# Kernel tuning notes

Measured on AMD Instinct MI355X. Metric: run time of the kernel, lower is better.

The kernel has to match this reference:

```python
import jax, jax.numpy as jnp
import numpy as np

B, L, D = 16384, 50, 64      # nodes, history length, embed_dim
NU, NI, NR = 100000, 100000, 5


def setup_inputs() -> dict:
    key = jax.random.key(0)
    ks = jax.random.split(key, 16)
    s = 0.05
    return {
        "nodes": jax.random.randint(ks[0], (B,), 0, NU),
        "history_uv": jax.random.randint(ks[1], (B, L), 0, NI),
        "history_r": jax.random.randint(ks[2], (B, L), 0, NR),
        "v2e_w": jax.random.normal(ks[3], (NI, D), jnp.float32) * s,
        "u2e_w": jax.random.normal(ks[4], (NU, D), jnp.float32) * s,
        "r2e_w": jax.random.normal(ks[5], (NR, D), jnp.float32) * s,
        "w_r1_w": jax.random.normal(ks[6], (2 * D, D), jnp.float32) * s,
        "w_r1_b": jnp.zeros((D,), jnp.float32),
        "w_r2_w": jax.random.normal(ks[7], (D, D), jnp.float32) * s,
        "w_r2_b": jnp.zeros((D,), jnp.float32),
        "att1_w": jax.random.normal(ks[8], (2 * D, D), jnp.float32) * s,
        "att1_b": jnp.zeros((D,), jnp.float32),
        "att2_w": jax.random.normal(ks[9], (D, D), jnp.float32) * s,
        "att2_b": jnp.zeros((D,), jnp.float32),
        "att3_w": jax.random.normal(ks[10], (D, 1), jnp.float32) * s,
        "att3_b": jnp.zeros((1,), jnp.float32),
    }


def reference(nodes, history_uv, history_r, v2e_w, u2e_w, r2e_w,
              w_r1_w, w_r1_b, w_r2_w, w_r2_b,
              att1_w, att1_b, att2_w, att2_b, att3_w, att3_b):
    # Gather neighbor (item) and rating embeddings: [B, L, D]
    e_uv = v2e_w[history_uv]
    e_r = r2e_w[history_r]
    uv_rep = u2e_w[nodes]                      # [B, D] self (user) embedding
    # 2-layer MLP on concatenated (item, rating) embeddings
    x = jnp.concatenate([e_uv, e_r], axis=-1)  # [B, L, 2D]
    h = jax.nn.relu(x @ w_r1_w + w_r1_b)
    o_history = jax.nn.relu(h @ w_r2_w + w_r2_b)  # [B, L, D]
    # Attention over neighbors (GraphRec Attention, dropout off in eval)
    a = jnp.concatenate(
        [o_history, jnp.broadcast_to(uv_rep[:, None, :], o_history.shape)], axis=-1)
    a = jax.nn.relu(a @ att1_w + att1_b)
    a = jax.nn.relu(a @ att2_w + att2_b)
    logits = (a @ att3_w + att3_b)[..., 0]     # [B, L]
    att = jax.nn.softmax(logits, axis=-1)      # softmax over history dim
    # Attention-weighted sum of neighbor representations
    return jnp.einsum('bl,bld->bd', att, o_history)  # [B, D]
```

## Files before the change

kernel.cpp:

```cpp
#include <hip/hip_runtime.h>
#include <math.h>

#define NB 16384
#define LH 50
#define D  64

#define TBF_OFF 49152
#define UB_OFF  65536
#define P1_OFF  4259840

typedef _Float16 half2v __attribute__((ext_vector_type(2)));
typedef _Float16 half8  __attribute__((ext_vector_type(8)));
typedef float    f32x16 __attribute__((ext_vector_type(16)));
typedef unsigned int u32;

#define MFMA(a, b, c) __builtin_amdgcn_mfma_f32_32x32x16_f16((a), (b), (c), 0, 0, 0)


__device__ __forceinline__ u32 pack2(float a, float b) {
    half2v h; h[0] = (_Float16)a; h[1] = (_Float16)b;
    return __builtin_bit_cast(u32, h);
}
__device__ __forceinline__ half8 mk8(u32 a, u32 b, u32 c, u32 d) {
    uint4 t = make_uint4(a, b, c, d);
    return __builtin_bit_cast(half8, t);
}
__device__ __forceinline__ half8 cvt8(const float* __restrict__ p) {
    float4 u = *(const float4*)p;
    float4 v = *(const float4*)(p + 4);
    return mk8(pack2(u.x, u.y), pack2(u.z, u.w), pack2(v.x, v.y), pack2(v.z, v.w));
}
__device__ __forceinline__ half8 addrelu8(half8 a, half8 r) {
    half8 s = a + r;
    #pragma unroll
    for (int j = 0; j < 8; ++j) s[j] = s[j] > (_Float16)0 ? s[j] : (_Float16)0;
    return s;
}

__device__ __forceinline__ void xform_tile(const f32x16& t, int hv, half8& f0, half8& f1) {
    u32 p[8], rp[8];
    #pragma unroll
    for (int q = 0; q < 8; ++q) p[q] = pack2(fmaxf(t[2*q], 0.f), fmaxf(t[2*q+1], 0.f));
    #pragma unroll
    for (int q = 0; q < 8; ++q) rp[q] = (u32)__shfl_xor((int)p[q], 32, 64);
    f0 = hv ? mk8(rp[2], rp[3], p[2], p[3]) : mk8(p[0], p[1], rp[0], rp[1]);
    f1 = hv ? mk8(rp[6], rp[7], p[6], p[7]) : mk8(p[4], p[5], rp[4], rp[5]);
}

__device__ __forceinline__ f32x16 ldbias(const float* __restrict__ tb, int hv, int mt) {
    const float4* p = (const float4*)tb + hv*8 + mt*4;
    f32x16 r;
    #pragma unroll
    for (int q = 0; q < 4; ++q) {
        float4 v = p[q];
        r[4*q] = v.x; r[4*q+1] = v.y; r[4*q+2] = v.z; r[4*q+3] = v.w;
    }
    return r;
}

__device__ __forceinline__ half8 mkw(const float* __restrict__ W, int ks, int mt,
                                     int hv, int m) {
    half8 r;
    #pragma unroll
    for (int j = 0; j < 8; ++j)
        r[j] = (_Float16)W[(ks*16 + hv*8 + j)*64 + mt*32 + m];
    return r;
}

__global__ __launch_bounds__(256) void prep_all(
    const int*   __restrict__ nodes,
    const float* __restrict__ v2e, const float* __restrict__ u2e,
    const float* __restrict__ r2e,
    const float* __restrict__ w1,  const float* __restrict__ b1,
    const float* __restrict__ w2,  const float* __restrict__ b2,
    const float* __restrict__ wa1, const float* __restrict__ ba1,
    const float* __restrict__ wa2, const float* __restrict__ ba2,
    const float* __restrict__ wa3,
    _Float16* __restrict__ wsh, float* __restrict__ tbf,
    float* __restrict__ UB, _Float16* __restrict__ P1h) {
    const int blk = blockIdx.x;
    const int lane = threadIdx.x & 63;
    const int n = lane & 31, hv = lane >> 5;

    if (blk < 782) {
        const int tile = blk*4 + (threadIdx.x >> 6);
        if (tile >= 3125) return;
        const int item = tile*32 + n;
        half8 bf[4];
        #pragma unroll
        for (int ks = 0; ks < 4; ++ks)
            bf[ks] = cvt8(v2e + (size_t)item*64 + ks*16 + hv*8);
        f32x16 a0, a1;
        #pragma unroll
        for (int q = 0; q < 16; ++q) { a0[q] = 0.f; a1[q] = 0.f; }
        #pragma unroll
        for (int ks = 0; ks < 4; ++ks) {
            a0 = MFMA(mkw(w1, ks, 0, hv, n), bf[ks], a0);
            a1 = MFMA(mkw(w1, ks, 1, hv, n), bf[ks], a1);
        }
        u32 dw[16];
        #pragma unroll
        for (int q = 0; q < 8; ++q) dw[q]     = pack2(a0[2*q], a0[2*q+1]);
        #pragma unroll
        for (int q = 0; q < 8; ++q) dw[8 + q] = pack2(a1[2*q], a1[2*q+1]);
        uint4* dst = (uint4*)(P1h + (size_t)item*64 + hv*32);
        dst[0] = make_uint4(dw[0],  dw[1],  dw[2],  dw[3]);
        dst[1] = make_uint4(dw[4],  dw[5],  dw[6],  dw[7]);
        dst[2] = make_uint4(dw[8],  dw[9],  dw[10], dw[11]);
        dst[3] = make_uint4(dw[12], dw[13], dw[14], dw[15]);
        return;
    }
    if (blk < 910) {
        const int tile = (blk - 782)*4 + (threadIdx.x >> 6);
        const int s = tile*32 + n;
        const int nid = nodes[s];
        half8 bf[4];
        #pragma unroll
        for (int ks = 0; ks < 4; ++ks)
            bf[ks] = cvt8(u2e + (size_t)nid*64 + ks*16 + hv*8);
        f32x16 a0, a1;
        #pragma unroll
        for (int q = 0; q < 16; ++q) {
            a0[q] = ba1[(q & 3) + 8*(q >> 2) + 4*hv];
            a1[q] = ba1[32 + (q & 3) + 8*(q >> 2) + 4*hv];
        }
        const float* wup = wa1 + 64*64;
        #pragma unroll
        for (int ks = 0; ks < 4; ++ks) {
            a0 = MFMA(mkw(wup, ks, 0, hv, n), bf[ks], a0);
            a1 = MFMA(mkw(wup, ks, 1, hv, n), bf[ks], a1);
        }
        float4* dst = (float4*)(UB + (size_t)s*64 + hv*32);
        #pragma unroll
        for (int q = 0; q < 4; ++q) {
            dst[q]     = make_float4(a0[4*q], a0[4*q+1], a0[4*q+2], a0[4*q+3]);
            dst[4 + q] = make_float4(a1[4*q], a1[4*q+1], a1[4*q+2], a1[4*q+3]);
        }
        return;
    }
    if (blk < 958) {
        const int idx = (blk - 910)*256 + threadIdx.x;
        const int j = idx & 7, l2 = (idx >> 3) & 63;
        const int hv2 = l2 >> 5, m31 = l2 & 31;
        const int f = (idx >> 9) & 7, ks = f & 3, mt = f >> 2;
        const int sec = idx >> 12;
        const int tau = ks*16 + hv2*8 + j;
        float v;
        if (sec == 0) {
            const int thv = (tau >> 5) & 1, tmt = (tau >> 4) & 1, i = tau & 15;
            const int feat = tmt*32 + (i & 3) + 8*(i >> 2) + 4*thv;
            v = w2[feat*64 + mt*32 + m31];
        }
        else if (sec == 1) v = wa1[tau*64 + mt*32 + m31];
        else               v = wa2[tau*64 + mt*32 + m31];
        wsh[idx] = (_Float16)v;
        return;
    }
    if (blk == 958) {
        if (threadIdx.x < 64) {
            const int t = threadIdx.x;
            const int thv = t >> 5, r = t & 31, mtt = r >> 4, i = r & 15;
            const int feat = mtt*32 + (i & 3) + 8*(i >> 2) + 4*thv;
            tbf[t]       = b2[feat];
            tbf[64 + t]  = ba2[feat];
            tbf[128 + t] = wa3[feat];
        }
        return;
    }
    {
        _Float16* R1h = (_Float16*)(tbf + 192);
        #pragma unroll 1
        for (int base = 0; base < 320; base += 256) {
            const int o = base + (int)threadIdx.x;
            if (o < 320) {
                const int rr = o >> 6, tt = o & 63;
                const int thv = tt >> 5, r5 = tt & 31, mtt = r5 >> 4, i = r5 & 15;
                const int feat = mtt*32 + (i & 3) + 8*(i >> 2) + 4*thv;
                float acc = b1[feat];
                for (int k = 0; k < 64; ++k)
                    acc += r2e[rr*64 + k] * w1[(64 + k)*64 + feat];
                R1h[rr*64 + tt] = (_Float16)acc;
            }
        }
    }
}

__global__ __launch_bounds__(256, 4) void uv_main(
    const int*   __restrict__ huv,
    const int*   __restrict__ hr,
    const _Float16* __restrict__ P1h,
    const float* __restrict__ UB,
    const _Float16* __restrict__ wsh,
    const float* __restrict__ tbf,
    float*       __restrict__ out) {
    __shared__ float4 stage[4][520];
    const int lane = threadIdx.x & 63;
    const int w = threadIdx.x >> 6;
    const int b = blockIdx.x * 4 + w;
    const int n = lane & 31, hv = lane >> 5;
    float4* const stg = stage[w];

    #define G8(base, f) (*(const half8*)(wsh + (base) + (size_t)((f)*64 + lane)*8))

    const int tg = lane >> 3;
    const int qq = lane & 7;
    int rowid[8];
    #pragma unroll
    for (int j = 0; j < 8; ++j) {
        int t = j*8 + tg; if (t > LH-1) t = LH-1;
        rowid[j] = huv[b*LH + t];
    }
    float4 c[8];
    #pragma unroll
    for (int j = 0; j < 8; ++j)
        c[j] = *(const float4*)(P1h + (size_t)rowid[j]*64 + qq*8);

    const _Float16* R1h = (const _Float16*)(tbf + 192);
    const int t1  = (32 + n < LH) ? 32 + n : LH - 1;
    const int ir0 = __builtin_nontemporal_load(hr + b*LH + n);
    const int ir1 = __builtin_nontemporal_load(hr + b*LH + t1);

    #pragma unroll
    for (int j = 0; j < 8; ++j) stg[qq*65 + j*8 + tg] = c[j];

    half8 bf[2][4];
    #pragma unroll
    for (int ks = 0; ks < 4; ++ks) {
        half8 r0 = *(const half8*)(R1h + ir0*64 + ks*16 + hv*8);
        half8 r1 = *(const half8*)(R1h + ir1*64 + ks*16 + hv*8);
        bf[0][ks] = addrelu8(*(const half8*)&stg[(2*ks + hv)*65 + n],      r0);
        bf[1][ks] = addrelu8(*(const half8*)&stg[(2*ks + hv)*65 + 32 + n], r1);
    }

    half8 of[2][4];
    #pragma unroll
    for (int mt = 0; mt < 2; ++mt) {
        f32x16 a0 = ldbias(tbf, hv, mt);
        f32x16 a1 = ldbias(tbf, hv, mt);
        #pragma unroll
        for (int ks = 0; ks < 4; ++ks) {
            half8 wv = G8(0, mt*4 + ks);
            a0 = MFMA(wv, bf[0][ks], a0);
            a1 = MFMA(wv, bf[1][ks], a1);
        }
        xform_tile(a0, hv, of[0][mt*2], of[0][mt*2 + 1]);
        xform_tile(a1, hv, of[1][mt*2], of[1][mt*2 + 1]);
    }

    const float* ubrow = UB + (size_t)b * 64;
    half8 af[2][4];
    #pragma unroll
    for (int mt = 0; mt < 2; ++mt) {
        f32x16 a0 = ldbias(ubrow, hv, mt);
        f32x16 a1 = ldbias(ubrow, hv, mt);
        #pragma unroll
        for (int ks = 0; ks < 4; ++ks) {
            half8 wv = G8(4096, mt*4 + ks);
            a0 = MFMA(wv, of[0][ks], a0);
            a1 = MFMA(wv, of[1][ks], a1);
        }
        xform_tile(a0, hv, af[0][mt*2], af[0][mt*2 + 1]);
        xform_tile(a1, hv, af[1][mt*2], af[1][mt*2 + 1]);
    }

    float lg0 = 0.f, lg1 = 0.f;
    #pragma unroll
    for (int mt = 0; mt < 2; ++mt) {
        f32x16 c0, c1v;
        {
            const f32x16 bc = ldbias(tbf + 64, hv, mt);
            half8 wv = G8(8192, mt*4 + 0);
            c0  = MFMA(wv, af[0][0], bc);
            c1v = MFMA(wv, af[1][0], bc);
        }
        #pragma unroll
        for (int ks = 1; ks < 4; ++ks) {
            half8 wv = G8(8192, mt*4 + ks);
            c0  = MFMA(wv, af[0][ks], c0);
            c1v = MFMA(wv, af[1][ks], c1v);
        }
        #pragma unroll
        for (int q = 0; q < 4; ++q) {
            float4 w3 = ((const float4*)(tbf + 128))[hv*8 + mt*4 + q];
            lg0 += fmaxf(c0[4*q], 0.f)*w3.x + fmaxf(c0[4*q+1], 0.f)*w3.y
                 + fmaxf(c0[4*q+2], 0.f)*w3.z + fmaxf(c0[4*q+3], 0.f)*w3.w;
            lg1 += fmaxf(c1v[4*q], 0.f)*w3.x + fmaxf(c1v[4*q+1], 0.f)*w3.y
                 + fmaxf(c1v[4*q+2], 0.f)*w3.z + fmaxf(c1v[4*q+3], 0.f)*w3.w;
        }
    }
    lg0 += __shfl_xor(lg0, 32, 64);
    lg1 += __shfl_xor(lg1, 32, 64);
    if (32 + n >= LH) lg1 = -1e30f;

    float mx = fmaxf(lg0, lg1);
    #pragma unroll
    for (int off = 16; off >= 1; off >>= 1) mx = fmaxf(mx, __shfl_xor(mx, off, 64));
    const float e0 = __expf(lg0 - mx);
    const float e1 = __expf(lg1 - mx);
    float s = e0 + e1;
    #pragma unroll
    for (int off = 16; off >= 1; off >>= 1) s += __shfl_xor(s, off, 64);
    const float at0 = e0 / s, at1 = e1 / s;

    float cur[32];
    #pragma unroll
    for (int ks = 0; ks < 4; ++ks)
        #pragma unroll
        for (int j = 0; j < 8; ++j)
            cur[ks*8 + j] = at0 * (float)of[0][ks][j] + at1 * (float)of[1][ks][j];
    #pragma unroll
    for (int k = 0; k < 5; ++k) {
        const int d = 1 << k, mybit = (lane >> k) & 1, half = 16 >> k;
        #pragma unroll
        for (int j2 = 0; j2 < 16; ++j2) {
            if (j2 < half) {
                float sel  = mybit ? cur[2*j2]     : cur[2*j2 + 1];
                float got  = __shfl_xor(sel, d, 64);
                float keep = mybit ? cur[2*j2 + 1] : cur[2*j2];
                cur[j2] = keep + got;
            }
        }
    }
    const int feat = ((lane >> 3) & 3)*16 + hv*8 + (lane & 7);
    __builtin_nontemporal_store(cur[0], out + (size_t)b * D + feat);
    #undef G8
}

extern "C" void kernel_launch(void* const* d_in, const int* in_sizes, int n_in,
                              void* d_out, int out_size, void* d_ws, size_t ws_size,
                              hipStream_t stream) {
    const int*   nodes      = (const int*)  d_in[0];
    const int*   history_uv = (const int*)  d_in[1];
    const int*   history_r  = (const int*)  d_in[2];
    const float* v2e        = (const float*)d_in[3];
    const float* u2e        = (const float*)d_in[4];
    const float* r2e        = (const float*)d_in[5];
    const float* w1         = (const float*)d_in[6];
    const float* b1         = (const float*)d_in[7];
    const float* w2         = (const float*)d_in[8];
    const float* b2         = (const float*)d_in[9];
    const float* wa1        = (const float*)d_in[10];
    const float* ba1        = (const float*)d_in[11];
    const float* wa2        = (const float*)d_in[12];
    const float* ba2        = (const float*)d_in[13];
    const float* wa3        = (const float*)d_in[14];
    float* out = (float*)d_out;

    _Float16* wsh = (_Float16*)d_ws;
    float*    tbf = (float*)((char*)d_ws + TBF_OFF);
    float*    UB  = (float*)((char*)d_ws + UB_OFF);
    _Float16* P1h = (_Float16*)((char*)d_ws + P1_OFF);

    prep_all<<<960, 256, 0, stream>>>(nodes, v2e, u2e, r2e, w1, b1, w2, b2,
                                      wa1, ba1, wa2, ba2, wa3, wsh, tbf, UB, P1h);
    uv_main<<<NB/4, 256, 0, stream>>>(history_uv, history_r,
                                      P1h, UB, wsh, tbf, out);
}
```

Measured before the change: 197.4 us.

## Stage weights and bias tables in LDS and gather item rows directly

Each block now copies the fp16 MLP/attention weights, bias/att3 vectors and the rating-embedding table into shared memory once, then reads them from LDS instead of global memory. The cooperative row gather through a padded LDS staging buffer is replaced by per-lane direct half8 loads of the P1 rows in MFMA fragment layout. Launch bounds are raised to 6 blocks per SM to allow more occupancy. The trade-off is a per-block prologue copy and a __syncthreads, plus less coalesced gather loads (16-byte per-lane reads scattered across rows) and tighter register limits.

```diff
diff --git a/kernel.cpp b/kernel.cpp
--- a/kernel.cpp
+++ b/kernel.cpp
@@ -47,7 +47,7 @@
     f1 = hv ? mk8(rp[6], rp[7], p[6], p[7]) : mk8(p[4], p[5], rp[4], rp[5]);
 }
 
-__device__ __forceinline__ f32x16 ldbias(const float* __restrict__ tb, int hv, int mt) {
+__device__ __forceinline__ f32x16 ldbias(const float* tb, int hv, int mt) {
     const float4* p = (const float4*)tb + hv*8 + mt*4;
     f32x16 r;
     #pragma unroll
@@ -185,7 +185,7 @@
     }
 }
 
-__global__ __launch_bounds__(256, 4) void uv_main(
+__global__ __launch_bounds__(256, 6) void uv_main(
     const int*   __restrict__ huv,
     const int*   __restrict__ hr,
     const _Float16* __restrict__ P1h,
@@ -193,50 +193,50 @@
     const _Float16* __restrict__ wsh,
     const float* __restrict__ tbf,
     float*       __restrict__ out) {
-    __shared__ float4 stage[4][520];
-    const int lane = threadIdx.x & 63;
-    const int w = threadIdx.x >> 6;
+    __shared__ _Float16 lw[12288];
+    __shared__ float    ltb[192];
+    __shared__ _Float16 lr1[320];
+    const int tid = threadIdx.x;
+
+    {
+        const uint4* src = (const uint4*)wsh;
+        uint4* dst = (uint4*)lw;
+        #pragma unroll
+        for (int i = 0; i < 6; ++i) dst[tid + 256*i] = src[tid + 256*i];
+        if (tid < 48) ((uint4*)ltb)[tid] = ((const uint4*)tbf)[tid];
+        if (tid < 40) ((uint4*)lr1)[tid] = ((const uint4*)(tbf + 192))[tid];
+    }
+    __syncthreads();
+
+    const int lane = tid & 63;
+    const int w = tid >> 6;
     const int b = blockIdx.x * 4 + w;
     const int n = lane & 31, hv = lane >> 5;
-    float4* const stg = stage[w];
-
-    #define G8(base, f) (*(const half8*)(wsh + (base) + (size_t)((f)*64 + lane)*8))
-
-    const int tg = lane >> 3;
-    const int qq = lane & 7;
-    int rowid[8];
-    #pragma unroll
-    for (int j = 0; j < 8; ++j) {
-        int t = j*8 + tg; if (t > LH-1) t = LH-1;
-        rowid[j] = huv[b*LH + t];
-    }
-    float4 c[8];
-    #pragma unroll
-    for (int j = 0; j < 8; ++j)
-        c[j] = *(const float4*)(P1h + (size_t)rowid[j]*64 + qq*8);
-
-    const _Float16* R1h = (const _Float16*)(tbf + 192);
-    const int t1  = (32 + n < LH) ? 32 + n : LH - 1;
-    const int ir0 = __builtin_nontemporal_load(hr + b*LH + n);
-    const int ir1 = __builtin_nontemporal_load(hr + b*LH + t1);
-
-    #pragma unroll
-    for (int j = 0; j < 8; ++j) stg[qq*65 + j*8 + tg] = c[j];
+
+    #define G8(base, f) (*(const half8*)(lw + (base) + ((f)*64 + lane)*8))
+
+    const int t1   = (32 + n < LH) ? 32 + n : LH - 1;
+    const int row0 = huv[b*LH + n];
+    const int row1 = huv[b*LH + t1];
+    const int ir0  = hr[b*LH + n];
+    const int ir1  = hr[b*LH + t1];
 
     half8 bf[2][4];
     #pragma unroll
     for (int ks = 0; ks < 4; ++ks) {
-        half8 r0 = *(const half8*)(R1h + ir0*64 + ks*16 + hv*8);
-        half8 r1 = *(const half8*)(R1h + ir1*64 + ks*16 + hv*8);
-        bf[0][ks] = addrelu8(*(const half8*)&stg[(2*ks + hv)*65 + n],      r0);
-        bf[1][ks] = addrelu8(*(const half8*)&stg[(2*ks + hv)*65 + 32 + n], r1);
+        half8 p0 = *(const half8*)(P1h + (size_t)row0*64 + ks*16 + hv*8);
+        half8 p1 = *(const half8*)(P1h + (size_t)row1*64 + ks*16 + hv*8);
+        half8 r0 = *(const half8*)(lr1 + ir0*64 + ks*16 + hv*8);
+        half8 r1 = *(const half8*)(lr1 + ir1*64 + ks*16 + hv*8);
+        bf[0][ks] = addrelu8(p0, r0);
+        bf[1][ks] = addrelu8(p1, r1);
     }
 
     half8 of[2][4];
     #pragma unroll
     for (int mt = 0; mt < 2; ++mt) {
-        f32x16 a0 = ldbias(tbf, hv, mt);
-        f32x16 a1 = ldbias(tbf, hv, mt);
+        f32x16 a0 = ldbias(ltb, hv, mt);
+        f32x16 a1 = ldbias(ltb, hv, mt);
         #pragma unroll
         for (int ks = 0; ks < 4; ++ks) {
             half8 wv = G8(0, mt*4 + ks);
@@ -268,7 +268,7 @@
     for (int mt = 0; mt < 2; ++mt) {
         f32x16 c0, c1v;
         {
-            const f32x16 bc = ldbias(tbf + 64, hv, mt);
+            const f32x16 bc = ldbias(ltb + 64, hv, mt);
             half8 wv = G8(8192, mt*4 + 0);
             c0  = MFMA(wv, af[0][0], bc);
             c1v = MFMA(wv, af[1][0], bc);
@@ -281,7 +281,7 @@
         }
         #pragma unroll
         for (int q = 0; q < 4; ++q) {
-            float4 w3 = ((const float4*)(tbf + 128))[hv*8 + mt*4 + q];
+            float4 w3 = ((const float4*)(ltb + 128))[hv*8 + mt*4 + q];
             lg0 += fmaxf(c0[4*q], 0.f)*w3.x + fmaxf(c0[4*q+1], 0.f)*w3.y
                  + fmaxf(c0[4*q+2], 0.f)*w3.z + fmaxf(c0[4*q+3], 0.f)*w3.w;
             lg1 += fmaxf(c1v[4*q], 0.f)*w3.x + fmaxf(c1v[4*q+1], 0.f)*w3.y
```

Result: slower. 250.3 us (+26.8%).
